# Kernel tuning notes

Measured on AMD Instinct MI355X. Metric: run time of the kernel, lower is better.

The kernel has to match this reference:

```python
import jax, jax.numpy as jnp
import numpy as np

B, S, L, D = 16, 1024, 512, 1024
H = 8
DH = D // H
WD = 256          # word/type embedding dim
VOCAB = 1000      # type vocab
NEG = -1e30


def setup_inputs() -> dict:
    key = jax.random.key(0)
    ks = jax.random.split(key, 16)
    inv = 1.0 / np.sqrt(D)
    return {
        "encoder_outs": jax.random.normal(ks[0], (B, S, D), dtype=jnp.float32),
        "to_sem": jax.random.randint(ks[1], (B, L), 0, S, dtype=jnp.int64),
        "to_sem_type": jax.random.randint(ks[2], (B, L), 0, VOCAB, dtype=jnp.int64),
        "sem_syn": jax.random.randint(ks[3], (B, S), 0, L + 1, dtype=jnp.int64),
        "wq": jax.random.normal(ks[4], (D, D), dtype=jnp.float32) * inv,
        "bq": jnp.zeros((D,), dtype=jnp.float32),
        "wk": jax.random.normal(ks[5], (D, D), dtype=jnp.float32) * inv,
        "bk": jnp.zeros((D,), dtype=jnp.float32),
        "wv": jax.random.normal(ks[6], (D, D), dtype=jnp.float32) * inv,
        "bv": jnp.zeros((D,), dtype=jnp.float32),
        "wo": jax.random.normal(ks[7], (D, D), dtype=jnp.float32) * inv,
        "bo": jnp.zeros((D,), dtype=jnp.float32),
        "type_emb": jax.random.normal(ks[8], (VOCAB, WD), dtype=jnp.float32),
        "w_proj": jax.random.normal(ks[9], (D, D + WD), dtype=jnp.float32) / np.sqrt(D + WD),
        "b_proj": jnp.zeros((D,), dtype=jnp.float32),
        "bias_root": jax.random.normal(ks[10], (1, 1, D), dtype=jnp.float32),
    }


def _forward(encoder_outs, to_sem, to_sem_type, sem_syn,
             wq, bq, wk, bk, wv, bv, wo, bo,
             type_emb, w_proj, b_proj, bias_root):
    bsz, len_sem = to_sem.shape
    src_len = encoder_outs.shape[1]

    # batch_index_select: gather the encoder states at semantic head positions
    sem_vec = jnp.take_along_axis(encoder_outs, to_sem[:, :, None], axis=1)  # [B,L,D]

    # Vectorized mask build (replaces the Python loop + scatter):
    # buf[b,i,j] = (sem_syn[b,j] == i+1) or (j == to_sem[b,i])
    ids = jnp.arange(1, len_sem + 1, dtype=sem_syn.dtype)
    aligned = sem_syn[:, None, :] == ids[None, :, None]                       # [B,L,S]
    self_pos = jnp.arange(src_len)[None, None, :] == to_sem[:, :, None]       # [B,L,S]
    allow = aligned | self_pos                                                # [B,L,S]

    # fairseq-style MHA: q scaled by head_dim**-0.5, in/out proj with bias
    q = (sem_vec @ wq.T + bq) * (DH ** -0.5)
    k = encoder_outs @ wk.T + bk
    v = encoder_outs @ wv.T + bv
    q = q.reshape(bsz, len_sem, H, DH)
    k = k.reshape(bsz, src_len, H, DH)
    v = v.reshape(bsz, src_len, H, DH)

    scores = jnp.einsum("blhd,bshd->bhls", q, k)                              # [B,H,L,S]
    scores = jnp.where(allow[:, None, :, :], scores, NEG)
    attn = jax.nn.softmax(scores, axis=-1)
    ctx = jnp.einsum("bhls,bshd->blhd", attn, v).reshape(bsz, len_sem, D)
    sem_vec = ctx @ wo.T + bo                                                 # [B,L,D]

    # arg/type embedding + concat + projection
    type_vec = type_emb[to_sem_type]                                          # [B,L,WD]
    embedding = jnp.concatenate([sem_vec, type_vec], axis=-1) @ w_proj.T + b_proj

    root = jnp.broadcast_to(bias_root, (bsz, 1, D))
    return embedding, jnp.concatenate([root, embedding], axis=1)


def reference(encoder_outs, to_sem, to_sem_type, sem_syn,
              wq, bq, wk, bk, wv, bv, wo, bo,
              type_emb, w_proj, b_proj, bias_root):
    return _forward(encoder_outs, to_sem, to_sem_type, sem_syn,
                    wq, bq, wk, bk, wv, bv, wo, bo,
                    type_emb, w_proj, b_proj, bias_root)
```

## Files before the change

### kernel.cpp

```cpp
#include <hip/hip_runtime.h>

typedef unsigned short u16;
typedef unsigned int   u32;
typedef unsigned long long u64;
typedef __bf16 bf16x8 __attribute__((ext_vector_type(8)));
typedef float  f32x4  __attribute__((ext_vector_type(4)));

#define B_  16
#define S_  1024
#define L_  512
#define D_  1024
#define H_  8
#define WD_ 256
#define KP_ (D_ + WD_)

__device__ __forceinline__ u16 f2bf(float f) {
    u32 u = __float_as_uint(f);
    return (u16)((u + 0x7FFFu + ((u >> 16) & 1u)) >> 16);
}
__device__ __forceinline__ float bf2f(u16 h) {
    return __uint_as_float(((u32)h) << 16);
}
__device__ __forceinline__ void gload16(const void* g, void* l) {
    __builtin_amdgcn_global_load_lds(
        (const __attribute__((address_space(1))) u32*)(unsigned long long)(g),
        (__attribute__((address_space(3))) u32*)(unsigned long long)(l),
        16, 0, 0);
}

__global__ __launch_bounds__(256) void prep_k(
    const float* __restrict__ enc,
    const float* __restrict__ wk, const float* __restrict__ wv,
    const float* __restrict__ wq, const float* __restrict__ te,
    const float* __restrict__ bk, const float* __restrict__ bv,
    const float* __restrict__ bq,
    const float* __restrict__ wo, const float* __restrict__ wproj,
    const float* __restrict__ bo, const float* __restrict__ bproj,
    u16* __restrict__ enc_bf, u16* __restrict__ wkvq, u16* __restrict__ te_bf,
    float* __restrict__ bkvq, u16* __restrict__ wot,
    u16* __restrict__ wp1, u16* __restrict__ wfin,
    float* __restrict__ beff, float qs)
{
    __shared__ float tile[64][65];
    const int bid = blockIdx.x;
    if (bid < 16384) {
        const int i = (bid * 256 + threadIdx.x) * 4;
        const float4 v = *(const float4*)(enc + i);
        ushort4 o;
        o.x = f2bf(v.x); o.y = f2bf(v.y); o.z = f2bf(v.z); o.w = f2bf(v.w);
        *(ushort4*)(enc_bf + i) = o;
    } else if (bid < 19456) {
        const int b2 = bid - 16384;
        const int plane = b2 >> 10;
        const int i = ((b2 & 1023) * 256 + threadIdx.x) * 4;
        const float* src = plane == 0 ? wk : (plane == 1 ? wv : wq);
        const float s = plane == 2 ? qs : 1.0f;
        const float4 v = *(const float4*)(src + i);
        ushort4 o;
        o.x = f2bf(v.x * s); o.y = f2bf(v.y * s); o.z = f2bf(v.z * s); o.w = f2bf(v.w * s);
        *(ushort4*)(wkvq + (size_t)plane * 1048576 + i) = o;
    } else if (bid < 19706) {
        const int i = ((bid - 19456) * 256 + threadIdx.x) * 4;
        if (i < 256000) {
            const float4 v = *(const float4*)(te + i);
            ushort4 o;
            o.x = f2bf(v.x); o.y = f2bf(v.y); o.z = f2bf(v.z); o.w = f2bf(v.w);
            *(ushort4*)(te_bf + i) = o;
        }
    } else if (bid < 19709) {
        const int i = (bid - 19706) * 1024 + threadIdx.x * 4;
        #pragma unroll
        for (int j = 0; j < 4; ++j) {
            const int idx = i + j;
            bkvq[idx] = (idx < 1024) ? bk[idx]
                      : (idx < 2048 ? bv[idx - 1024] : bq[idx - 2048] * qs);
        }
    } else if (bid < 19965) {
        const int cid = bid - 19709;
        const int t0 = (cid & 15) * 64;
        const int k0 = (cid >> 4) * 64;
        const int tr = threadIdx.x >> 4;
        const int tc = threadIdx.x & 15;
        #pragma unroll
        for (int i = 0; i < 4; ++i) {
            const int r = tr + i * 16;
            const float4 v = *(const float4*)(wo + (size_t)(t0 + r) * 1024 + k0 + tc * 4);
            tile[r][tc * 4 + 0] = v.x; tile[r][tc * 4 + 1] = v.y;
            tile[r][tc * 4 + 2] = v.z; tile[r][tc * 4 + 3] = v.w;
        }
        __syncthreads();
        #pragma unroll
        for (int i = 0; i < 4; ++i) {
            const int r = tr + i * 16;
            ushort4 o;
            o.x = f2bf(tile[tc * 4 + 0][r]);
            o.y = f2bf(tile[tc * 4 + 1][r]);
            o.z = f2bf(tile[tc * 4 + 2][r]);
            o.w = f2bf(tile[tc * 4 + 3][r]);
            *(ushort4*)(wot + (size_t)(k0 + r) * 1024 + t0 + tc * 4) = o;
        }
    } else if (bid < 21245) {
        const int i = ((bid - 19965) * 256 + threadIdx.x) * 4;
        const int n = i / 1280, c = i % 1280;
        const float4 v = *(const float4*)(wproj + i);
        ushort4 o;
        o.x = f2bf(v.x); o.y = f2bf(v.y); o.z = f2bf(v.z); o.w = f2bf(v.w);
        if (c < 1024) *(ushort4*)(wp1 + (size_t)n * 1024 + c) = o;
        else          *(ushort4*)(wfin + (size_t)n * 1280 + c) = o;
    } else {
        const int w = threadIdx.x >> 6, lane = threadIdx.x & 63;
        const int n = (bid - 21245) * 4 + w;
        const float* row = wproj + (size_t)n * 1280;
        float s = 0.f;
        for (int t = lane; t < 1024; t += 64) s += row[t] * bo[t];
        #pragma unroll
        for (int off = 32; off > 0; off >>= 1) s += __shfl_down(s, off);
        if (lane == 0) beff[n] = bproj[n] + s;
    }
}

template <int NT>
__global__ __launch_bounds__(512, 4) void mm8_k(
    const u16* __restrict__ A, const u16* __restrict__ W,
    const float* __restrict__ bias,
    u16* __restrict__ o0, u16* __restrict__ o1,
    int K, int ntn)
{
    __shared__ alignas(16) u16 lds[24576];
    const int tid  = threadIdx.x;
    const int w    = tid >> 6;
    const int lane = tid & 63;
    const int l15  = lane & 15;
    const int lk   = lane >> 4;
    const int wr   = w >> 2;
    const int wc   = w & 3;

    const int nwg = gridDim.x;
    const int bid = blockIdx.x;
    const int e   = (bid & 7) * (nwg >> 3) + (bid >> 3);
    const int bm0 = (e / ntn) * 128;
    const int bn0 = (e % ntn) * 256;

    const int kc_l = (lane & 3) ^ ((lane >> 3) & 3);
    const size_t aA  = (size_t)(bm0 + w * 16 + (lane >> 2)) * K + kc_l * 8;
    const size_t bB0 = (size_t)(bn0 + w * 32 + (lane >> 2)) * K + kc_l * 8;
    const size_t bB1 = (size_t)(bn0 + w * 32 + 16 + (lane >> 2)) * K + kc_l * 8;

#define STAGE(t) { u16* s = lds + ((t) & 1) * 12288;                   \
    gload16(A + aA  + (size_t)(t) * 32, s + w * 512);                  \
    gload16(W + bB0 + (size_t)(t) * 32, s + 4096 + w * 1024);          \
    gload16(W + bB1 + (size_t)(t) * 32, s + 4096 + w * 1024 + 512); }

    const int slot8 = (lk ^ ((l15 >> 1) & 3)) * 8;
    const int aoff = wr * 2048 + l15 * 32 + slot8;
    const int boff = 4096 + wc * 2048 + l15 * 32 + slot8;

    f32x4 acc[4][4] = {};

    STAGE(0);

    for (int t = 0; t < NT; ++t) {
        if (t + 1 < NT) {
            STAGE(t + 1);
            asm volatile("s_waitcnt vmcnt(3)" ::: "memory");
        } else {
            asm volatile("s_waitcnt vmcnt(0)" ::: "memory");
        }
        __builtin_amdgcn_sched_barrier(0);
        __builtin_amdgcn_s_barrier();

        const u16* sa = lds + (t & 1) * 12288 + aoff;
        const u16* sb = lds + (t & 1) * 12288 + boff;
        bf16x8 af[4], bfr[4];
        #pragma unroll
        for (int nf = 0; nf < 4; ++nf) bfr[nf] = *(const bf16x8*)(sb + nf * 512);
        #pragma unroll
        for (int mf = 0; mf < 4; ++mf) af[mf] = *(const bf16x8*)(sa + mf * 512);
        __builtin_amdgcn_s_setprio(1);
        #pragma unroll
        for (int mf = 0; mf < 4; ++mf)
            #pragma unroll
            for (int nf = 0; nf < 4; ++nf)
                acc[mf][nf] = __builtin_amdgcn_mfma_f32_16x16x32_bf16(af[mf], bfr[nf], acc[mf][nf], 0, 0, 0);
        __builtin_amdgcn_s_setprio(0);
        __builtin_amdgcn_s_barrier();
    }
#undef STAGE

    const int plane = bn0 >> 10;
    u16* outp = plane == 0 ? o0 : o1;
    const int cip0 = (bn0 & 1023) + wc * 64;
    const int colg = bn0 + wc * 64 + l15;
    float bsv[4];
    #pragma unroll
    for (int nf = 0; nf < 4; ++nf) bsv[nf] = bias[colg + nf * 16];
    const int erow = lane >> 3;
    const int echk = lane & 7;
    u16* wlds = lds + w * 2304;

    #pragma unroll
    for (int mf = 0; mf < 4; ++mf) {
        u16* pat = wlds + (mf & 1) * 1152;
        #pragma unroll
        for (int nf = 0; nf < 4; ++nf) {
            #pragma unroll
            for (int r = 0; r < 4; ++r) {
                const float val = acc[mf][nf][r] + bsv[nf];
                const float pv = __shfl_xor(val, 1, 64);
                if ((l15 & 1) == 0) {
                    const u32 pk = (u32)f2bf(val) | ((u32)f2bf(pv) << 16);
                    *(u32*)(pat + (lk * 4 + r) * 72 + nf * 16 + l15) = pk;
                }
            }
        }
        asm volatile("s_waitcnt lgkmcnt(0)" ::: "memory");
        __builtin_amdgcn_sched_barrier(0);
        #pragma unroll
        for (int j2 = 0; j2 < 2; ++j2) {
            const int rr = j2 * 8 + erow;
            const uint4 vv = *(const uint4*)(pat + rr * 72 + echk * 8);
            const int grow = bm0 + wr * 64 + mf * 16 + rr;
            *(uint4*)(outp + (size_t)grow * 1024 + cip0 + echk * 8) = vv;
        }
    }
}

__global__ __launch_bounds__(256) void qw_k(
    const u16* __restrict__ enc_bf, const u16* __restrict__ wq_w,
    const float* __restrict__ bq_s, u16* __restrict__ q_out,
    const u16* __restrict__ wp1, const u16* __restrict__ wot,
    u16* __restrict__ wfin, const int* __restrict__ to_sem)
{
    __shared__ alignas(16) u16 lds[32768];

    const int bid  = blockIdx.x;
    const bool isQ = bid < 512;
    const int tid  = threadIdx.x;
    const int wid  = tid >> 6;
    const int lane = tid & 63;
    const int l15  = lane & 15;
    const int lk   = lane >> 4;

    const u16* pA; const u16* pW; const float* pB; u16* pO; int ostride; int e;
    if (isQ) {
        e = (bid & 7) * 64 + (bid >> 3);
        pA = enc_bf; pW = wq_w; pB = bq_s; pO = q_out; ostride = 1024;
    } else {
        const int b2 = bid - 512;
        e = (b2 & 7) * 8 + (b2 >> 3);
        pA = wp1; pW = wot; pB = nullptr; pO = wfin; ostride = 1280;
    }
    const int bm0 = (e >> 3) * 128;
    const int bn0 = (e & 7) * 128;

    const int kc_l = (lane & 3) ^ ((lane >> 3) & 3);
    long ga[2], gw[2];
    #pragma unroll
    for (int i = 0; i < 2; ++i) {
        const int row = wid * 32 + i * 16 + (lane >> 2);
        const int m = bm0 + row;
        ga[i] = isQ ? ((long)(m >> 9) * S_ + to_sem[m]) * D_ + kc_l * 8
                    : (long)m * 1024 + kc_l * 8;
        gw[i] = (long)(bn0 + row) * 1024 + kc_l * 8;
    }

#define QSTAGE(t) { const int k0t = (t) * 32;                              \
    u16* d  = lds + ((t) & 3) * 8192 + wid * 1024;                         \
    u16* db = d + 4096;                                                    \
    gload16(pA + ga[0] + k0t, d);                                          \
    gload16(pA + ga[1] + k0t, d + 512);                                    \
    gload16(pW + gw[0] + k0t, db);                                         \
    gload16(pW + gw[1] + k0t, db + 512); }

    f32x4 acc[4][4] = {};

    const int moff = (wid >> 1) * 64;
    const int noff = (wid & 1) * 64;
    const int rslot = (lk ^ ((l15 >> 1) & 3)) * 8;
    const int aoff = (moff + l15) * 32 + rslot;
    const int boff = 4096 + (noff + l15) * 32 + rslot;

    QSTAGE(0); QSTAGE(1); QSTAGE(2);
    asm volatile("s_waitcnt vmcnt(8)" ::: "memory");
    __builtin_amdgcn_sched_barrier(0);
    __builtin_amdgcn_s_barrier();

    for (int t = 0; t < 32; ++t) {
        const u16* sa = lds + (t & 3) * 8192 + aoff;
        const u16* sb = lds + (t & 3) * 8192 + boff;
        bf16x8 af[4], bfr[4];
        #pragma unroll
        for (int j = 0; j < 4; ++j) bfr[j] = *(const bf16x8*)(sb + j * 512);
        #pragma unroll
        for (int i = 0; i < 4; ++i) af[i] = *(const bf16x8*)(sa + i * 512);
        if (t + 3 < 32) QSTAGE(t + 3);
        __builtin_amdgcn_s_setprio(1);
        #pragma unroll
        for (int i = 0; i < 4; ++i)
            #pragma unroll
            for (int j = 0; j < 4; ++j)
                acc[i][j] = __builtin_amdgcn_mfma_f32_16x16x32_bf16(af[i], bfr[j], acc[i][j], 0, 0, 0);
        __builtin_amdgcn_s_setprio(0);
        if (t < 29)      { asm volatile("s_waitcnt vmcnt(8)" ::: "memory"); }
        else if (t == 29){ asm volatile("s_waitcnt vmcnt(4)" ::: "memory"); }
        else if (t == 30){ asm volatile("s_waitcnt vmcnt(0)" ::: "memory"); }
        __builtin_amdgcn_sched_barrier(0);
        __builtin_amdgcn_s_barrier();
    }
#undef QSTAGE

    #pragma unroll
    for (int j = 0; j < 4; ++j) {
        const int col = bn0 + noff + j * 16 + l15;
        const float bj = pB ? pB[col] : 0.f;
        #pragma unroll
        for (int i = 0; i < 4; ++i) {
            const int mrow = bm0 + moff + i * 16 + lk * 4;
            #pragma unroll
            for (int r = 0; r < 4; ++r)
                pO[(long)(mrow + r) * ostride + col] = f2bf(acc[i][j][r] + bj);
        }
    }
}

__global__ __launch_bounds__(256) void fin_k(
    const u16* __restrict__ A, const u16* __restrict__ W,
    const float* __restrict__ bias,
    float* __restrict__ Yf, float* __restrict__ Y2,
    const int* __restrict__ gidx, const u16* __restrict__ aux,
    const float* __restrict__ broot)
{
    constexpr int NT = 40;
    __shared__ alignas(16) u16 lds[32768];

    const int bid = blockIdx.x;
    if (bid >= 512) {
        const int i = (bid - 512) * 256 + threadIdx.x;
        const int b = i >> 10, d = i & 1023;
        Y2[(size_t)b * (L_ + 1) * D_ + d] = broot[d];
        return;
    }

    const int tid  = threadIdx.x;
    const int wid  = tid >> 6;
    const int lane = tid & 63;
    const int l15  = lane & 15;
    const int lk   = lane >> 4;

    const int e   = (bid & 7) * 64 + (bid >> 3);
    const int bm0 = (e >> 3) * 128;
    const int bn0 = (e & 7) * 128;

    const int kc_l = (lane & 3) ^ ((lane >> 3) & 3);
    long ga[2], gw[2], gt[2];
    #pragma unroll
    for (int i = 0; i < 2; ++i) {
        const int row = wid * 32 + i * 16 + (lane >> 2);
        const int m = bm0 + row;
        ga[i] = (long)m * D_ + kc_l * 8;
        gt[i] = (long)gidx[m] * WD_ + kc_l * 8;
        gw[i] = (long)(bn0 + row) * KP_ + kc_l * 8;
    }

#define FSTAGE(t) { const int k0t = (t) * 32;                              \
    u16* d  = lds + ((t) & 3) * 8192 + wid * 1024;                         \
    u16* db = d + 4096;                                                    \
    if (k0t >= D_) {                                                       \
        gload16(aux + gt[0] + (k0t - D_), d);                              \
        gload16(aux + gt[1] + (k0t - D_), d + 512);                        \
    } else {                                                               \
        gload16(A + ga[0] + k0t, d);                                       \
        gload16(A + ga[1] + k0t, d + 512);                                 \
    }                                                                      \
    gload16(W + gw[0] + k0t, db);                                          \
    gload16(W + gw[1] + k0t, db + 512); }

    f32x4 acc[4][4] = {};

    const int moff = (wid >> 1) * 64;
    const int noff = (wid & 1) * 64;
    const int rslot = (lk ^ ((l15 >> 1) & 3)) * 8;
    const int aoff = (moff + l15) * 32 + rslot;
    const int boff = 4096 + (noff + l15) * 32 + rslot;

    FSTAGE(0); FSTAGE(1); FSTAGE(2);
    asm volatile("s_waitcnt vmcnt(8)" ::: "memory");
    __builtin_amdgcn_sched_barrier(0);
    __builtin_amdgcn_s_barrier();

    for (int t = 0; t < NT; ++t) {
        const u16* sa = lds + (t & 3) * 8192 + aoff;
        const u16* sb = lds + (t & 3) * 8192 + boff;
        bf16x8 af[4], bfr[4];
        #pragma unroll
        for (int j = 0; j < 4; ++j) bfr[j] = *(const bf16x8*)(sb + j * 512);
        #pragma unroll
        for (int i = 0; i < 4; ++i) af[i] = *(const bf16x8*)(sa + i * 512);
        if (t + 3 < NT) FSTAGE(t + 3);
        __builtin_amdgcn_s_setprio(1);
        #pragma unroll
        for (int i = 0; i < 4; ++i)
            #pragma unroll
            for (int j = 0; j < 4; ++j)
                acc[i][j] = __builtin_amdgcn_mfma_f32_16x16x32_bf16(af[i], bfr[j], acc[i][j], 0, 0, 0);
        __builtin_amdgcn_s_setprio(0);
        if (t < NT - 3)      { asm volatile("s_waitcnt vmcnt(8)" ::: "memory"); }
        else if (t == NT - 3){ asm volatile("s_waitcnt vmcnt(4)" ::: "memory"); }
        else if (t == NT - 2){ asm volatile("s_waitcnt vmcnt(0)" ::: "memory"); }
        __builtin_amdgcn_sched_barrier(0);
        __builtin_amdgcn_s_barrier();
    }
#undef FSTAGE

    #pragma unroll
    for (int j = 0; j < 4; ++j) {
        const int col = bn0 + noff + j * 16 + l15;
        const float bj = bias[col];
        #pragma unroll
        for (int i = 0; i < 4; ++i) {
            const int mrow = bm0 + moff + i * 16 + lk * 4;
            #pragma unroll
            for (int r = 0; r < 4; ++r) {
                const float val = acc[i][j][r] + bj;
                const long m = mrow + r;
                Yf[m * (long)D_ + col] = val;
                const long bb = m >> 9, ll = m & 511;
                Y2[((bb * (L_ + 1)) + ll + 1) * (long)D_ + col] = val;
            }
        }
    }
}

__global__ __launch_bounds__(256) void attn_k(
    const u16* __restrict__ kb, const u16* __restrict__ vb,
    const int* __restrict__ sem_syn, const int* __restrict__ to_sem,
    const u16* __restrict__ qf, u16* __restrict__ ctx)
{
    __shared__ int   list[S_];
    __shared__ float sc[H_][S_];
    __shared__ int   wcnt[16];

    const int bl  = blockIdx.x;
    const int b   = bl >> 9;
    const int l   = bl & 511;
    const int tid = threadIdx.x;
    const int wvi = tid >> 6;
    const int ln  = tid & 63;

    const int tosem = to_sem[bl];
    const ushort4 qu = *(const ushort4*)(qf + (size_t)bl * D_ + tid * 4);
    const float4 qv = make_float4(bf2f(qu.x), bf2f(qu.y), bf2f(qu.z), bf2f(qu.w));

    bool al[4];
    #pragma unroll
    for (int j = 0; j < 4; ++j) {
        const int s = tid * 4 + j;
        const int a = sem_syn[b * S_ + s];
        al[j] = (a == l + 1) || (s == tosem);
    }
    u64 msk[4];
    #pragma unroll
    for (int j = 0; j < 4; ++j) msk[j] = __ballot(al[j]);
    if (ln == 0) {
        #pragma unroll
        for (int j = 0; j < 4; ++j) wcnt[wvi * 4 + j] = __popcll(msk[j]);
    }
    __syncthreads();
    int mybase[4];
    {
        int tot = 0;
        #pragma unroll
        for (int i2 = 0; i2 < 16; ++i2) {
            const int c2 = wcnt[i2];
            #pragma unroll
            for (int j2 = 0; j2 < 4; ++j2)
                if (i2 == wvi * 4 + j2) mybase[j2] = tot;
            tot += c2;
        }
    }
    const u64 lmlt = (1ull << ln) - 1ull;
    #pragma unroll
    for (int j = 0; j < 4; ++j)
        if (al[j]) list[mybase[j] + __popcll(msk[j] & lmlt)] = tid * 4 + j;
    int n = 0;
    #pragma unroll
    for (int i2 = 0; i2 < 16; ++i2) n += wcnt[i2];
    __syncthreads();

    const int g = tid >> 5;
    const int lane = tid & 31;
    for (int i = 0; i < n; ++i) {
        const u16* krow = kb + ((size_t)b * S_ + list[i]) * D_;
        const ushort4 ku = *(const ushort4*)(krow + tid * 4);
        float p = bf2f(ku.x) * qv.x + bf2f(ku.y) * qv.y + bf2f(ku.z) * qv.z + bf2f(ku.w) * qv.w;
        #pragma unroll
        for (int off = 16; off > 0; off >>= 1) p += __shfl_down(p, off, 32);
        if (lane == 0) sc[g][i] = p;
    }
    __syncthreads();

    float mx = -3.0e38f;
    for (int i = lane; i < n; i += 32) mx = fmaxf(mx, sc[g][i]);
    #pragma unroll
    for (int off = 16; off > 0; off >>= 1) mx = fmaxf(mx, __shfl_xor(mx, off, 32));
    float sum = 0.f;
    for (int i = lane; i < n; i += 32) {
        const float e = expf(sc[g][i] - mx);
        sc[g][i] = e;
        sum += e;
    }
    #pragma unroll
    for (int off = 16; off > 0; off >>= 1) sum += __shfl_xor(sum, off, 32);
    const float inv = 1.0f / sum;
    __syncthreads();

    float4 a4 = make_float4(0.f, 0.f, 0.f, 0.f);
    for (int i = 0; i < n; ++i) {
        const float wgt = sc[g][i] * inv;
        const u16* vrow = vb + ((size_t)b * S_ + list[i]) * D_;
        const ushort4 vu = *(const ushort4*)(vrow + tid * 4);
        a4.x = fmaf(wgt, bf2f(vu.x), a4.x);
        a4.y = fmaf(wgt, bf2f(vu.y), a4.y);
        a4.z = fmaf(wgt, bf2f(vu.z), a4.z);
        a4.w = fmaf(wgt, bf2f(vu.w), a4.w);
    }
    ushort4 o;
    o.x = f2bf(a4.x); o.y = f2bf(a4.y); o.z = f2bf(a4.z); o.w = f2bf(a4.w);
    *(ushort4*)(ctx + (size_t)bl * D_ + tid * 4) = o;
}

extern "C" void kernel_launch(void* const* d_in, const int* in_sizes, int n_in,
                              void* d_out, int out_size, void* d_ws, size_t ws_size,
                              hipStream_t stream)
{
    const float* enc    = (const float*)d_in[0];
    const int*   to_sem = (const int*)  d_in[1];
    const int*   tstype = (const int*)  d_in[2];
    const int*   semsyn = (const int*)  d_in[3];
    const float* wq = (const float*)d_in[4];
    const float* bq = (const float*)d_in[5];
    const float* wk = (const float*)d_in[6];
    const float* bk = (const float*)d_in[7];
    const float* wv = (const float*)d_in[8];
    const float* bv = (const float*)d_in[9];
    const float* wo = (const float*)d_in[10];
    const float* bo = (const float*)d_in[11];
    const float* temb  = (const float*)d_in[12];
    const float* wproj = (const float*)d_in[13];
    const float* bproj = (const float*)d_in[14];
    const float* broot = (const float*)d_in[15];

    float* out1 = (float*)d_out;
    float* out2 = out1 + (size_t)B_ * L_ * D_;

    unsigned char* ws = (unsigned char*)d_ws;
    u16*   enc_bf = (u16*)(ws);
    u16*   k_bf   = (u16*)(ws + (32ull << 20));
    u16*   wkvq   = (u16*)(ws + (64ull << 20));
    u16*   wot    = (u16*)(ws + (70ull << 20));
    u16*   wp1    = (u16*)(ws + (72ull << 20));
    u16*   wfin   = (u16*)(ws + (74ull << 20));
    float* beff   = (float*)(ws + (77ull << 20));
    float* bkvq   = (float*)(ws + (77ull << 20) + 8192);
    u16*   ctx_bf = (u16*)(ws + (78ull << 20));
    u16*   te_bf  = (u16*)(ws + (94ull << 20));

    u16* v_bf = (u16*)d_out;
    u16* q_bf = (u16*)((unsigned char*)d_out + (32ull << 20));

    const float qscale = 0.08838834764831845f;
    dim3 blk(256);

    prep_k<<<dim3(21501), blk, 0, stream>>>(
        enc, wk, wv, wq, temb, bk, bv, bq, wo, wproj, bo, bproj,
        enc_bf, wkvq, te_bf, bkvq, wot, wp1, wfin, beff, qscale);

    mm8_k<32><<<dim3(1024), dim3(512), 0, stream>>>(
        enc_bf, wkvq, bkvq, k_bf, v_bf, 1024, 8);

    qw_k<<<dim3(576), blk, 0, stream>>>(
        enc_bf, wkvq + 2097152, bkvq + 2048, q_bf, wp1, wot, wfin, to_sem);

    attn_k<<<dim3(B_ * L_), blk, 0, stream>>>(k_bf, v_bf, semsyn, to_sem, q_bf, ctx_bf);

    fin_k<<<dim3(576), blk, 0, stream>>>(
        ctx_bf, wfin, beff, out1, out2, tstype, te_bf, broot);
}
```

Baseline: 214.1 us.

## Enlarge KV GEMM tile to 256x256 with 1024 threads and 4-stage LDS pipeline

The K/V projection GEMM now uses 256x256 output tiles computed by 16 waves, instead of 128x256 tiles with 8 waves. The grid is halved to match. Double buffering is replaced by a 4-deep LDS ring prefetched three tiles ahead, with the next stage issued after the fragment reads, to cut global traffic per FLOP and hide load latency. The cost is 128KB of LDS per block, which allows only one block per CU, and the finer-grained waitcnt handling at the tail is more fragile.

Result: no change. 211.8 us (median of 2 runs) (-1.1%).

```diff
diff --git a/kernel.cpp b/kernel.cpp
--- a/kernel.cpp
+++ b/kernel.cpp
@@ -120,13 +120,13 @@
 }
 
 template <int NT>
-__global__ __launch_bounds__(512, 4) void mm8_k(
+__global__ __launch_bounds__(1024, 4) void mm8_k(
     const u16* __restrict__ A, const u16* __restrict__ W,
     const float* __restrict__ bias,
     u16* __restrict__ o0, u16* __restrict__ o1,
     int K, int ntn)
 {
-    __shared__ alignas(16) u16 lds[24576];
+    __shared__ alignas(16) u16 lds[65536];
     const int tid  = threadIdx.x;
     const int w    = tid >> 6;
     const int lane = tid & 63;
@@ -138,44 +138,44 @@
     const int nwg = gridDim.x;
     const int bid = blockIdx.x;
     const int e   = (bid & 7) * (nwg >> 3) + (bid >> 3);
-    const int bm0 = (e / ntn) * 128;
+    const int bm0 = (e / ntn) * 256;
     const int bn0 = (e % ntn) * 256;
 
     const int kc_l = (lane & 3) ^ ((lane >> 3) & 3);
-    const size_t aA  = (size_t)(bm0 + w * 16 + (lane >> 2)) * K + kc_l * 8;
-    const size_t bB0 = (size_t)(bn0 + w * 32 + (lane >> 2)) * K + kc_l * 8;
-    const size_t bB1 = (size_t)(bn0 + w * 32 + 16 + (lane >> 2)) * K + kc_l * 8;
-
-#define STAGE(t) { u16* s = lds + ((t) & 1) * 12288;                   \
-    gload16(A + aA  + (size_t)(t) * 32, s + w * 512);                  \
-    gload16(W + bB0 + (size_t)(t) * 32, s + 4096 + w * 1024);          \
-    gload16(W + bB1 + (size_t)(t) * 32, s + 4096 + w * 1024 + 512); }
-
-    const int slot8 = (lk ^ ((l15 >> 1) & 3)) * 8;
-    const int aoff = wr * 2048 + l15 * 32 + slot8;
-    const int boff = 4096 + wc * 2048 + l15 * 32 + slot8;
+    const u16* gsrc = (w < 8) ? A : W;
+    const int rbase = (w < 8) ? bm0 : bn0;
+    size_t src[2];
+    #pragma unroll
+    for (int i = 0; i < 2; ++i) {
+        const int row = (w & 7) * 32 + i * 16 + (lane >> 2);
+        src[i] = (size_t)(rbase + row) * K + kc_l * 8;
+    }
+    const int dstA = ((w < 8) ? 0 : 8192) + (w & 7) * 1024;
+
+#define STAGE(t) { u16* d = lds + ((t) & 3) * 16384 + dstA;            \
+    gload16(gsrc + src[0] + (size_t)(t) * 32, d);                      \
+    gload16(gsrc + src[1] + (size_t)(t) * 32, d + 512); }
+
+    const int rslot = (lk ^ ((l15 >> 1) & 3)) * 8;
+    const int aoff = (wr * 64 + l15) * 32 + rslot;
+    const int boff = 8192 + (wc * 64 + l15) * 32 + rslot;
 
     f32x4 acc[4][4] = {};
 
-    STAGE(0);
+    STAGE(0); STAGE(1); STAGE(2);
+    asm volatile("s_waitcnt vmcnt(4)" ::: "memory");
+    __builtin_amdgcn_sched_barrier(0);
+    __builtin_amdgcn_s_barrier();
 
     for (int t = 0; t < NT; ++t) {
-        if (t + 1 < NT) {
-            STAGE(t + 1);
-            asm volatile("s_waitcnt vmcnt(3)" ::: "memory");
-        } else {
-            asm volatile("s_waitcnt vmcnt(0)" ::: "memory");
-        }
-        __builtin_amdgcn_sched_barrier(0);
-        __builtin_amdgcn_s_barrier();
-
-        const u16* sa = lds + (t & 1) * 12288 + aoff;
-        const u16* sb = lds + (t & 1) * 12288 + boff;
+        const u16* sa = lds + (t & 3) * 16384 + aoff;
+        const u16* sb = lds + (t & 3) * 16384 + boff;
         bf16x8 af[4], bfr[4];
         #pragma unroll
         for (int nf = 0; nf < 4; ++nf) bfr[nf] = *(const bf16x8*)(sb + nf * 512);
         #pragma unroll
         for (int mf = 0; mf < 4; ++mf) af[mf] = *(const bf16x8*)(sa + mf * 512);
+        if (t + 3 < NT) STAGE(t + 3);
         __builtin_amdgcn_s_setprio(1);
         #pragma unroll
         for (int mf = 0; mf < 4; ++mf)
@@ -183,6 +183,10 @@
             for (int nf = 0; nf < 4; ++nf)
                 acc[mf][nf] = __builtin_amdgcn_mfma_f32_16x16x32_bf16(af[mf], bfr[nf], acc[mf][nf], 0, 0, 0);
         __builtin_amdgcn_s_setprio(0);
+        if (t < NT - 3)      { asm volatile("s_waitcnt vmcnt(4)" ::: "memory"); }
+        else if (t == NT - 3){ asm volatile("s_waitcnt vmcnt(2)" ::: "memory"); }
+        else if (t == NT - 2){ asm volatile("s_waitcnt vmcnt(0)" ::: "memory"); }
+        __builtin_amdgcn_sched_barrier(0);
         __builtin_amdgcn_s_barrier();
     }
 #undef STAGE
@@ -575,7 +579,7 @@
         enc, wk, wv, wq, temb, bk, bv, bq, wo, wproj, bo, bproj,
         enc_bf, wkvq, te_bf, bkvq, wot, wp1, wfin, beff, qscale);
 
-    mm8_k<32><<<dim3(1024), dim3(512), 0, stream>>>(
+    mm8_k<32><<<dim3(512), dim3(1024), 0, stream>>>(
         enc_bf, wkvq, bkvq, k_bf, v_bf, 1024, 8);
 
     qw_k<<<dim3(576), blk, 0, stream>>>(
```
